# Kernel tuning notes

Measured on AMD Instinct MI355X. Metric: run time of the kernel, lower is better.

## Reference

```python
import jax, jax.numpy as jnp
import numpy as np
from jax.ops import segment_sum, segment_max

B, L, D, H, DK, NL, V, FF = 8, 256, 256, 8, 32, 4, 2048, 1024
N = B * L
EPS = 1e-5


def _ln(x, g, b):
    m = jnp.mean(x, -1, keepdims=True)
    v = jnp.var(x, -1, keepdims=True)
    return (x - m) * jax.lax.rsqrt(v + EPS) * g + b


def setup_inputs() -> dict:
    key = jax.random.key(0)
    ks = list(jax.random.split(key, 16))
    # causal decoder-decoder edges, sorted by destination (DGL 'dd' eids)
    dst_seq = np.repeat(np.arange(L), np.arange(L) + 1)
    src_seq = np.concatenate([np.arange(j + 1) for j in range(L)])
    src = jnp.asarray(np.concatenate([src_seq + b * L for b in range(B)]), jnp.int32)
    dst = jnp.asarray(np.concatenate([dst_seq + b * L for b in range(B)]), jnp.int32)
    tokens = jax.random.randint(ks[0], (N,), 0, V)
    positions = jnp.tile(jnp.arange(L), B)  # tgt[1]
    s = 0.02
    nrm = lambda k, sh: jax.random.normal(k, sh, jnp.float32) * s
    return {
        'tokens': tokens, 'positions': positions, 'src': src, 'dst': dst,
        'value_tab': nrm(ks[1], (V, D)),
        'coord_tab': nrm(ks[2], (3, D)),
        'pos_tab': nrm(ks[3], (L, D)),
        'ln1_g': jnp.ones((NL, D), jnp.float32), 'ln1_b': jnp.zeros((NL, D), jnp.float32),
        'Wq': nrm(ks[4], (NL, D, D)), 'Wk': nrm(ks[5], (NL, D, D)),
        'Wv': nrm(ks[6], (NL, D, D)), 'Wo': nrm(ks[7], (NL, D, D)),
        'ln2_g': jnp.ones((NL, D), jnp.float32), 'ln2_b': jnp.zeros((NL, D), jnp.float32),
        'W1': nrm(ks[8], (NL, D, FF)), 'b1': jnp.zeros((NL, FF), jnp.float32),
        'W2': nrm(ks[9], (NL, FF, D)), 'b2': jnp.zeros((NL, D), jnp.float32),
        'lnf_g': jnp.ones((D,), jnp.float32), 'lnf_b': jnp.zeros((D,), jnp.float32),
        'Wgen': nrm(ks[10], (D, V)), 'bgen': jnp.zeros((V,), jnp.float32),
    }


def reference(tokens, positions, src, dst, value_tab, coord_tab, pos_tab,
              ln1_g, ln1_b, Wq, Wk, Wv, Wo, ln2_g, ln2_b,
              W1, b1, W2, b2, lnf_g, lnf_b, Wgen, bgen):
    # embeddings: value*sqrt(d) + coord(pos%3) + pos(pos//3)
    x = value_tab[tokens] * jnp.sqrt(jnp.float32(D)) \
        + coord_tab[positions % 3] + pos_tab[positions // 3]
    inv_sqrt_dk = 1.0 / jnp.sqrt(jnp.float32(DK))
    for i in range(NL):
        # pre_func: layernorm + qkv projection, split heads
        xn = _ln(x, ln1_g[i], ln1_b[i])
        q = (xn @ Wq[i]).reshape(N, H, DK)
        k = (xn @ Wk[i]).reshape(N, H, DK)
        v = (xn @ Wv[i]).reshape(N, H, DK)
        # apply_edges(u_dot_v): per-edge, per-head score
        score = jnp.einsum('ehd,ehd->eh', k[src], q[dst]) * inv_sqrt_dk  # [E,H]
        # edge_softmax over edges grouped by destination node
        m = jax.lax.stop_gradient(
            segment_max(score, dst, num_segments=N, indices_are_sorted=True))
        a = jnp.exp(score - m[dst])
        denom = segment_sum(a, dst, num_segments=N, indices_are_sorted=True)
        alpha = a / denom[dst]  # [E,H]
        # send_and_recv(u_mul_e -> sum): softmax-weighted aggregation
        z = segment_sum(v[src] * alpha[..., None], dst,
                        num_segments=N, indices_are_sorted=True).reshape(N, D)
        # post_func: output proj + residual, then FFN sublayer
        x = x + z @ Wo[i]
        xn2 = _ln(x, ln2_g[i], ln2_b[i])
        x = x + (jax.nn.relu(xn2 @ W1[i] + b1[i]) @ W2[i] + b2[i])
    x = _ln(x, lnf_g, lnf_b)
    return jax.nn.log_softmax(x @ Wgen + bgen, axis=-1)  # generator
```

## Files before the change

### kernel.cpp

```cpp
#include <hip/hip_runtime.h>
#include <hip/hip_bf16.h>
#include <math.h>

constexpr int B_ = 8, L_ = 256, D_ = 256, H_ = 8, DK_ = 32, NL_ = 4, V_ = 2048, FF_ = 1024;
constexpr int N_ = B_ * L_;
constexpr float EPS_ = 1e-5f;

typedef short bf16x8 __attribute__((ext_vector_type(8)));
typedef float f32x4 __attribute__((ext_vector_type(4)));
typedef _Float16 f16x4 __attribute__((ext_vector_type(4)));

__device__ __forceinline__ short f2b(float f) {
    union { __hip_bfloat16 h; short s; } u;
    u.h = __float2bfloat16(f);
    return u.s;
}

__global__ void embed_kernel(const int* __restrict__ tokens, const int* __restrict__ positions,
                             const float* __restrict__ vtab, const float* __restrict__ ctab,
                             const float* __restrict__ ptab, float* __restrict__ x) {
    int n = blockIdx.x, d = threadIdx.x;
    int tok = tokens[n], p = positions[n];
    x[n * D_ + d] = vtab[tok * D_ + d] * 16.0f + ctab[(p % 3) * D_ + d] + ptab[(p / 3) * D_ + d];
}

__global__ void ln_kernel(const float* __restrict__ x, const float* __restrict__ g,
                          const float* __restrict__ b, short* __restrict__ out) {
    __shared__ float r1[4], r2[4], mv[2];
    int n = blockIdx.x, t = threadIdx.x;
    float v = x[n * D_ + t];
    float s1 = v, s2 = v * v;
#pragma unroll
    for (int off = 32; off; off >>= 1) {
        s1 += __shfl_down(s1, off, 64);
        s2 += __shfl_down(s2, off, 64);
    }
    int w = t >> 6;
    if ((t & 63) == 0) { r1[w] = s1; r2[w] = s2; }
    __syncthreads();
    if (t == 0) {
        float a = r1[0] + r1[1] + r1[2] + r1[3];
        float c = r2[0] + r2[1] + r2[2] + r2[3];
        float mean = a * (1.0f / D_);
        float var = c * (1.0f / D_) - mean * mean;
        mv[0] = mean;
        mv[1] = rsqrtf(var + EPS_);
    }
    __syncthreads();
    out[n * D_ + t] = f2b((v - mv[0]) * mv[1] * g[t] + b[t]);
}

__global__ void transpose_w(const float* __restrict__ src, short* __restrict__ dst, int K, int Nn) {
    __shared__ float tile[32][33];
    int n0 = blockIdx.x * 32, k0 = blockIdx.y * 32;
    size_t base = (size_t)blockIdx.z * K * Nn;
    src += base;
    dst += base;
    int tx = threadIdx.x, ty = threadIdx.y;
#pragma unroll
    for (int i = 0; i < 32; i += 8)
        tile[ty + i][tx] = src[(size_t)(k0 + ty + i) * Nn + n0 + tx];
    __syncthreads();
#pragma unroll
    for (int i = 0; i < 32; i += 8)
        dst[(size_t)(n0 + ty + i) * K + k0 + tx] = f2b(tile[tx][ty + i]);
}

template <int EPI, bool HAS_BIAS>
__device__ __forceinline__ void gemm_body(const short* __restrict__ A, const short* __restrict__ Bt,
                                          const float* __restrict__ bias, float* __restrict__ Cf,
                                          short* __restrict__ Cb, int M, int K, int Nout,
                                          int kbeg, int kend, int kz) {
    __shared__ short As[64][48];
    __shared__ short Bs[64][48];
    int t = threadIdx.x;
    int m0 = blockIdx.x * 64, n0 = blockIdx.y * 64;
    int sr = t >> 2, sc = (t & 3) * 8;
    int lane = t & 63, w = t >> 6;
    int mo = (w & 1) * 32, no = (w >> 1) * 32;
    int quad = lane >> 4, r = lane & 15;
    f32x4 acc00 = {}, acc01 = {}, acc10 = {}, acc11 = {};
    const short* Ap = &A[(size_t)(m0 + sr) * K + sc];
    const short* Bp = &Bt[(size_t)(n0 + sr) * K + sc];
    for (int k0 = kbeg; k0 < kend; k0 += 32) {
        int4 av = *(const int4*)(Ap + k0);
        int4 bv = *(const int4*)(Bp + k0);
        __syncthreads();
        *(int4*)&As[sr][sc] = av;
        *(int4*)&Bs[sr][sc] = bv;
        __syncthreads();
        bf16x8 a0 = *(const bf16x8*)&As[mo + r][quad * 8];
        bf16x8 a1 = *(const bf16x8*)&As[mo + 16 + r][quad * 8];
        bf16x8 b0 = *(const bf16x8*)&Bs[no + r][quad * 8];
        bf16x8 b1 = *(const bf16x8*)&Bs[no + 16 + r][quad * 8];
        acc00 = __builtin_amdgcn_mfma_f32_16x16x32_bf16(a0, b0, acc00, 0, 0, 0);
        acc01 = __builtin_amdgcn_mfma_f32_16x16x32_bf16(a0, b1, acc01, 0, 0, 0);
        acc10 = __builtin_amdgcn_mfma_f32_16x16x32_bf16(a1, b0, acc10, 0, 0, 0);
        acc11 = __builtin_amdgcn_mfma_f32_16x16x32_bf16(a1, b1, acc11, 0, 0, 0);
    }
#pragma unroll
    for (int i = 0; i < 2; ++i) {
#pragma unroll
        for (int j = 0; j < 2; ++j) {
            f32x4 acc = (i == 0) ? (j == 0 ? acc00 : acc01) : (j == 0 ? acc10 : acc11);
            int col = n0 + no + j * 16 + r;
            float bval = HAS_BIAS ? bias[col] : 0.f;
#pragma unroll
            for (int p = 0; p < 4; ++p) {
                int row = m0 + mo + i * 16 + quad * 4 + p;
                float v = acc[p];
                if (EPI == 0) {
                    Cf[(size_t)row * Nout + col] = v;
                } else if (EPI == 1) {
                    Cb[(size_t)row * Nout + col] = f2b(fmaxf(v + bval, 0.f));
                } else if (EPI == 2) {
                    float add = v + ((HAS_BIAS && kz == 0) ? bval : 0.f);
                    atomicAdd(&Cf[(size_t)row * Nout + col], add);
                } else if (EPI == 3) {
                    Cf[(size_t)row * Nout + col] = v + bval;
                } else if (EPI == 4) {
                    Cb[(size_t)row * Nout + col] = f2b(v);
                } else {
                    ((_Float16*)Cb)[(size_t)row * Nout + col] = (_Float16)v;
                }
            }
        }
    }
}

__global__ __launch_bounds__(256) void gemm_qkv(const short* __restrict__ A, const short* __restrict__ wq,
                                                const short* __restrict__ wk, const short* __restrict__ wv,
                                                short* __restrict__ q, short* __restrict__ k,
                                                short* __restrict__ v, int M, int K, int Nout) {
    if (blockIdx.z == 0)
        gemm_body<4, false>(A, wq, nullptr, nullptr, q, M, K, Nout, 0, K, 0);
    else if (blockIdx.z == 1)
        gemm_body<4, false>(A, wk, nullptr, nullptr, k, M, K, Nout, 0, K, 0);
    else
        gemm_body<5, false>(A, wv, nullptr, nullptr, v, M, K, Nout, 0, K, 0);
}

template <int SPLITK, bool HAS_BIAS>
__global__ __launch_bounds__(256) void gemm_accum(const short* __restrict__ A, const short* __restrict__ Bt,
                                                  const float* __restrict__ bias, float* __restrict__ C,
                                                  int M, int K, int Nout) {
    int Kp = K / SPLITK;
    int kz = blockIdx.z;
    gemm_body<2, HAS_BIAS>(A, Bt, bias, C, nullptr, M, K, Nout, kz * Kp, kz * Kp + Kp, kz);
}

__global__ __launch_bounds__(256) void gemm_biasrelu_bf16(const short* __restrict__ A,
                                                          const short* __restrict__ Bt,
                                                          const float* __restrict__ bias,
                                                          short* __restrict__ C, int M, int K, int Nout) {
    gemm_body<1, true>(A, Bt, bias, nullptr, C, M, K, Nout, 0, K, 0);
}

__global__ __launch_bounds__(256) void gemm_bias(const short* __restrict__ A, const short* __restrict__ Bt,
                                                 const float* __restrict__ bias, float* __restrict__ C,
                                                 int M, int K, int Nout) {
    gemm_body<3, true>(A, Bt, bias, C, nullptr, M, K, Nout, 0, K, 0);
}

__global__ __launch_bounds__(64) void attn_kernel(const short* __restrict__ q,
                                                  const short* __restrict__ k,
                                                  const _Float16* __restrict__ v,
                                                  short* __restrict__ z) {
    int blk = blockIdx.x;
    int bh = blk & 63;
    int qt = 15 - (blk >> 6);
    int b = bh >> 3, h = bh & 7;
    int lane = threadIdx.x;
    int r = lane & 15, quad = lane >> 4;
    int row0 = b * L_;

    bf16x8 qf = *(const bf16x8*)&q[(size_t)(row0 + qt * 16 + r) * D_ + h * DK_ + quad * 8];
    f32x4 O0 = {}, O1 = {};
    float mA = -1e30f, den = 0.f;
    int nk = qt + 1;

    bf16x8 kf = *(const bf16x8*)&k[(size_t)(row0 + r) * D_ + h * DK_ + quad * 8];
    f16x4 va, vb;
    {
        const _Float16* vp = v + (size_t)(row0 + quad * 4) * D_ + h * DK_;
#pragma unroll
        for (int i = 0; i < 4; ++i) {
            va[i] = vp[(size_t)i * D_ + r];
            vb[i] = vp[(size_t)i * D_ + 16 + r];
        }
    }
    for (int kt = 0; kt < nk; ++kt) {
        bf16x8 kf_n = kf;
        f16x4 va_n = va, vb_n = vb;
        if (kt + 1 < nk) {
            kf_n = *(const bf16x8*)&k[(size_t)(row0 + (kt + 1) * 16 + r) * D_ + h * DK_ + quad * 8];
            const _Float16* vp = v + (size_t)(row0 + (kt + 1) * 16 + quad * 4) * D_ + h * DK_;
#pragma unroll
            for (int i = 0; i < 4; ++i) {
                va_n[i] = vp[(size_t)i * D_ + r];
                vb_n[i] = vp[(size_t)i * D_ + 16 + r];
            }
        }
        f32x4 zero = {};
        f32x4 s = __builtin_amdgcn_mfma_f32_16x16x32_bf16(kf, qf, zero, 0, 0, 0);
#pragma unroll
        for (int i2 = 0; i2 < 4; ++i2) s[i2] *= 0.17677669529663687f;
        if (kt == qt) {
#pragma unroll
            for (int i2 = 0; i2 < 4; ++i2)
                if (quad * 4 + i2 > r) s[i2] = -1e30f;
        }
        float tmax = fmaxf(fmaxf(s[0], s[1]), fmaxf(s[2], s[3]));
        tmax = fmaxf(tmax, __shfl_xor(tmax, 16, 64));
        tmax = fmaxf(tmax, __shfl_xor(tmax, 32, 64));
        float mn = fmaxf(mA, tmax);
        float alpha = __expf(mA - mn);
        mA = mn;
        float p0 = __expf(s[0] - mn), p1 = __expf(s[1] - mn);
        float p2 = __expf(s[2] - mn), p3 = __expf(s[3] - mn);
        float ts = (p0 + p1) + (p2 + p3);
        ts += __shfl_xor(ts, 16, 64);
        ts += __shfl_xor(ts, 32, 64);
        den = den * alpha + ts;
        f16x4 pf;
        pf[0] = (_Float16)p0; pf[1] = (_Float16)p1; pf[2] = (_Float16)p2; pf[3] = (_Float16)p3;
        float al[4];
#pragma unroll
        for (int i2 = 0; i2 < 4; ++i2) al[i2] = __shfl(alpha, quad * 4 + i2, 64);
#pragma unroll
        for (int i2 = 0; i2 < 4; ++i2) { O0[i2] *= al[i2]; O1[i2] *= al[i2]; }
        O0 = __builtin_amdgcn_mfma_f32_16x16x16f16(pf, va, O0, 0, 0, 0);
        O1 = __builtin_amdgcn_mfma_f32_16x16x16f16(pf, vb, O1, 0, 0, 0);
        kf = kf_n; va = va_n; vb = vb_n;
    }
#pragma unroll
    for (int i2 = 0; i2 < 4; ++i2) {
        float inv = 1.0f / __shfl(den, quad * 4 + i2, 64);
        int rowz = row0 + qt * 16 + quad * 4 + i2;
        z[(size_t)rowz * D_ + h * DK_ + r] = f2b(O0[i2] * inv);
        z[(size_t)rowz * D_ + h * DK_ + 16 + r] = f2b(O1[i2] * inv);
    }
}

__global__ void lsm_kernel(float* __restrict__ logits) {
    __shared__ float rm[4], rs[4];
    int row = blockIdx.x, t = threadIdx.x;
    float* p = logits + (size_t)row * V_;
    float vals[8];
    float mx = -INFINITY;
#pragma unroll
    for (int i = 0; i < 8; ++i) {
        vals[i] = p[t + i * 256];
        mx = fmaxf(mx, vals[i]);
    }
#pragma unroll
    for (int off = 32; off; off >>= 1) mx = fmaxf(mx, __shfl_xor(mx, off, 64));
    int w = t >> 6;
    if ((t & 63) == 0) rm[w] = mx;
    __syncthreads();
    mx = fmaxf(fmaxf(rm[0], rm[1]), fmaxf(rm[2], rm[3]));
    float s = 0.f;
#pragma unroll
    for (int i = 0; i < 8; ++i) s += __expf(vals[i] - mx);
#pragma unroll
    for (int off = 32; off; off >>= 1) s += __shfl_xor(s, off, 64);
    if ((t & 63) == 0) rs[w] = s;
    __syncthreads();
    s = rs[0] + rs[1] + rs[2] + rs[3];
    float lse = mx + logf(s);
#pragma unroll
    for (int i = 0; i < 8; ++i) p[t + i * 256] = vals[i] - lse;
}

extern "C" void kernel_launch(void* const* d_in, const int* in_sizes, int n_in,
                              void* d_out, int out_size, void* d_ws, size_t ws_size,
                              hipStream_t stream) {
    const int* tokens = (const int*)d_in[0];
    const int* positions = (const int*)d_in[1];
    const float* vtab = (const float*)d_in[4];
    const float* ctab = (const float*)d_in[5];
    const float* ptab = (const float*)d_in[6];
    const float* ln1_g = (const float*)d_in[7];
    const float* ln1_b = (const float*)d_in[8];
    const float* Wq = (const float*)d_in[9];
    const float* Wk = (const float*)d_in[10];
    const float* Wv = (const float*)d_in[11];
    const float* Wo = (const float*)d_in[12];
    const float* ln2_g = (const float*)d_in[13];
    const float* ln2_b = (const float*)d_in[14];
    const float* W1 = (const float*)d_in[15];
    const float* b1 = (const float*)d_in[16];
    const float* W2 = (const float*)d_in[17];
    const float* b2 = (const float*)d_in[18];
    const float* lnf_g = (const float*)d_in[19];
    const float* lnf_b = (const float*)d_in[20];
    const float* Wgen = (const float*)d_in[21];
    const float* bgen = (const float*)d_in[22];

    char* p = (char*)d_ws;
    float* x = (float*)p;      p += (size_t)N_ * D_ * 4;
    short* qb = (short*)p;     p += (size_t)N_ * D_ * 4;
    short* kb = (short*)p;     p += (size_t)N_ * D_ * 4;
    short* vbh = (short*)p;    p += (size_t)N_ * D_ * 4;
    short* xnb = (short*)p;    p += (size_t)N_ * D_ * 2;
    short* zbb = (short*)p;    p += (size_t)N_ * D_ * 2;
    short* hbb = (short*)p;    p += (size_t)N_ * FF_ * 2;
    short* wqT = (short*)p;    p += (size_t)NL_ * D_ * D_ * 2;
    short* wkT = (short*)p;    p += (size_t)NL_ * D_ * D_ * 2;
    short* wvT = (short*)p;    p += (size_t)NL_ * D_ * D_ * 2;
    short* woT = (short*)p;    p += (size_t)NL_ * D_ * D_ * 2;
    short* w1T = (short*)p;    p += (size_t)NL_ * D_ * FF_ * 2;
    short* w2T = (short*)p;    p += (size_t)NL_ * FF_ * D_ * 2;
    short* wgT = (short*)p;    p += (size_t)D_ * V_ * 2;
    float* out = (float*)d_out;

    dim3 tb(32, 8);
    transpose_w<<<dim3(8, 8, NL_), tb, 0, stream>>>(Wq, wqT, D_, D_);
    transpose_w<<<dim3(8, 8, NL_), tb, 0, stream>>>(Wk, wkT, D_, D_);
    transpose_w<<<dim3(8, 8, NL_), tb, 0, stream>>>(Wv, wvT, D_, D_);
    transpose_w<<<dim3(8, 8, NL_), tb, 0, stream>>>(Wo, woT, D_, D_);
    transpose_w<<<dim3(32, 8, NL_), tb, 0, stream>>>(W1, w1T, D_, FF_);
    transpose_w<<<dim3(8, 32, NL_), tb, 0, stream>>>(W2, w2T, FF_, D_);
    transpose_w<<<dim3(64, 8, 1), tb, 0, stream>>>(Wgen, wgT, D_, V_);

    embed_kernel<<<N_, 256, 0, stream>>>(tokens, positions, vtab, ctab, ptab, x);
    dim3 gQKV(N_ / 64, D_ / 64, 3);
    dim3 gWo(N_ / 64, D_ / 64, 2);
    dim3 gW1(N_ / 64, FF_ / 64);
    dim3 gW2(N_ / 64, D_ / 64, 4);
    dim3 gGen(N_ / 64, V_ / 64);
    for (int i = 0; i < NL_; ++i) {
        ln_kernel<<<N_, 256, 0, stream>>>(x, ln1_g + i * D_, ln1_b + i * D_, xnb);
        gemm_qkv<<<gQKV, 256, 0, stream>>>(xnb, wqT + (size_t)i * D_ * D_, wkT + (size_t)i * D_ * D_,
                                           wvT + (size_t)i * D_ * D_, qb, kb, vbh, N_, D_, D_);
        attn_kernel<<<B_ * H_ * 16, 64, 0, stream>>>(qb, kb, (const _Float16*)vbh, zbb);
        gemm_accum<2, false><<<gWo, 256, 0, stream>>>(zbb, woT + (size_t)i * D_ * D_, nullptr, x, N_, D_, D_);
        ln_kernel<<<N_, 256, 0, stream>>>(x, ln2_g + i * D_, ln2_b + i * D_, xnb);
        gemm_biasrelu_bf16<<<gW1, 256, 0, stream>>>(xnb, w1T + (size_t)i * D_ * FF_, b1 + (size_t)i * FF_,
                                                    hbb, N_, D_, FF_);
        gemm_accum<4, true><<<gW2, 256, 0, stream>>>(hbb, w2T + (size_t)i * FF_ * D_, b2 + (size_t)i * D_,
                                                     x, N_, FF_, D_);
    }
    ln_kernel<<<N_, 256, 0, stream>>>(x, lnf_g, lnf_b, xnb);
    gemm_bias<<<gGen, 256, 0, stream>>>(xnb, wgT, bgen, out, N_, D_, V_);
    lsm_kernel<<<N_, 256, 0, stream>>>(out);
}
```

Before: 335.1 us.

## Stage full K-chunks in registers for GEMMs and fuse weight transposes

The GEMM body now loads its whole K slice (up to 256 elements) into registers up front and stages it into wider LDS tiles in 128-wide phases. This replaces a 32-wide step that needed two barriers per step, so the loop drops many syncs and global-load latency stalls. The seven transpose launches become one combined kernel, and the embedding is fused with the first layernorm. The cost is more registers and more LDS per block, which may lower occupancy.

```diff
diff --git a/kernel.cpp b/kernel.cpp
--- a/kernel.cpp
+++ b/kernel.cpp
@@ -16,19 +16,16 @@
     return u.s;
 }
 
-__global__ void embed_kernel(const int* __restrict__ tokens, const int* __restrict__ positions,
-                             const float* __restrict__ vtab, const float* __restrict__ ctab,
-                             const float* __restrict__ ptab, float* __restrict__ x) {
-    int n = blockIdx.x, d = threadIdx.x;
-    int tok = tokens[n], p = positions[n];
-    x[n * D_ + d] = vtab[tok * D_ + d] * 16.0f + ctab[(p % 3) * D_ + d] + ptab[(p / 3) * D_ + d];
-}
-
-__global__ void ln_kernel(const float* __restrict__ x, const float* __restrict__ g,
-                          const float* __restrict__ b, short* __restrict__ out) {
+__global__ void embed_ln_kernel(const int* __restrict__ tokens, const int* __restrict__ positions,
+                                const float* __restrict__ vtab, const float* __restrict__ ctab,
+                                const float* __restrict__ ptab, const float* __restrict__ g,
+                                const float* __restrict__ b, float* __restrict__ x,
+                                short* __restrict__ out) {
     __shared__ float r1[4], r2[4], mv[2];
     int n = blockIdx.x, t = threadIdx.x;
-    float v = x[n * D_ + t];
+    int tok = tokens[n], p = positions[n];
+    float v = vtab[tok * D_ + t] * 16.0f + ctab[(p % 3) * D_ + t] + ptab[(p / 3) * D_ + t];
+    x[n * D_ + t] = v;
     float s1 = v, s2 = v * v;
 #pragma unroll
     for (int off = 32; off; off >>= 1) {
@@ -50,29 +47,87 @@
     out[n * D_ + t] = f2b((v - mv[0]) * mv[1] * g[t] + b[t]);
 }
 
-__global__ void transpose_w(const float* __restrict__ src, short* __restrict__ dst, int K, int Nn) {
+__global__ void ln_kernel(const float* __restrict__ x, const float* __restrict__ g,
+                          const float* __restrict__ b, short* __restrict__ out) {
+    __shared__ float r1[4], r2[4], mv[2];
+    int n = blockIdx.x, t = threadIdx.x;
+    float v = x[n * D_ + t];
+    float s1 = v, s2 = v * v;
+#pragma unroll
+    for (int off = 32; off; off >>= 1) {
+        s1 += __shfl_down(s1, off, 64);
+        s2 += __shfl_down(s2, off, 64);
+    }
+    int w = t >> 6;
+    if ((t & 63) == 0) { r1[w] = s1; r2[w] = s2; }
+    __syncthreads();
+    if (t == 0) {
+        float a = r1[0] + r1[1] + r1[2] + r1[3];
+        float c = r2[0] + r2[1] + r2[2] + r2[3];
+        float mean = a * (1.0f / D_);
+        float var = c * (1.0f / D_) - mean * mean;
+        mv[0] = mean;
+        mv[1] = rsqrtf(var + EPS_);
+    }
+    __syncthreads();
+    out[n * D_ + t] = f2b((v - mv[0]) * mv[1] * g[t] + b[t]);
+}
+
+__global__ void transpose_all(const float* __restrict__ Wq, const float* __restrict__ Wk,
+                              const float* __restrict__ Wv, const float* __restrict__ Wo,
+                              const float* __restrict__ W1, const float* __restrict__ W2,
+                              const float* __restrict__ Wgen,
+                              short* __restrict__ wqT, short* __restrict__ wkT,
+                              short* __restrict__ wvT, short* __restrict__ woT,
+                              short* __restrict__ w1T, short* __restrict__ w2T,
+                              short* __restrict__ wgT) {
     __shared__ float tile[32][33];
-    int n0 = blockIdx.x * 32, k0 = blockIdx.y * 32;
-    size_t base = (size_t)blockIdx.z * K * Nn;
-    src += base;
-    dst += base;
-    int tx = threadIdx.x, ty = threadIdx.y;
+    int id = blockIdx.x;
+    const float* src;
+    short* dst;
+    int K, Nn, tx, ty;
+    if (id < 1024) {
+        int m = id >> 8, rem = id & 255, layer = rem >> 6, tt = rem & 63;
+        K = 256; Nn = 256; tx = tt & 7; ty = tt >> 3;
+        size_t off = (size_t)layer * 256 * 256;
+        if (m == 0) { src = Wq + off; dst = wqT + off; }
+        else if (m == 1) { src = Wk + off; dst = wkT + off; }
+        else if (m == 2) { src = Wv + off; dst = wvT + off; }
+        else { src = Wo + off; dst = woT + off; }
+    } else if (id < 2048) {
+        int rem = id - 1024, layer = rem >> 8, tt = rem & 255;
+        K = 256; Nn = 1024; tx = tt & 31; ty = tt >> 5;
+        size_t off = (size_t)layer * 256 * 1024;
+        src = W1 + off; dst = w1T + off;
+    } else if (id < 3072) {
+        int rem = id - 2048, layer = rem >> 8, tt = rem & 255;
+        K = 1024; Nn = 256; tx = tt & 7; ty = tt >> 3;
+        size_t off = (size_t)layer * 1024 * 256;
+        src = W2 + off; dst = w2T + off;
+    } else {
+        int tt = id - 3072;
+        K = 256; Nn = 2048; tx = tt & 63; ty = tt >> 6;
+        src = Wgen; dst = wgT;
+    }
+    int n0 = tx * 32, k0 = ty * 32;
+    int x_ = threadIdx.x, y_ = threadIdx.y;
 #pragma unroll
     for (int i = 0; i < 32; i += 8)
-        tile[ty + i][tx] = src[(size_t)(k0 + ty + i) * Nn + n0 + tx];
+        tile[y_ + i][x_] = src[(size_t)(k0 + y_ + i) * Nn + n0 + x_];
     __syncthreads();
 #pragma unroll
     for (int i = 0; i < 32; i += 8)
-        dst[(size_t)(n0 + ty + i) * K + k0 + tx] = f2b(tile[tx][ty + i]);
-}
-
-template <int EPI, bool HAS_BIAS>
+        dst[(size_t)(n0 + y_ + i) * K + k0 + x_] = f2b(tile[x_][y_ + i]);
+}
+
+template <int EPI, bool HAS_BIAS, int NC>
 __device__ __forceinline__ void gemm_body(const short* __restrict__ A, const short* __restrict__ Bt,
                                           const float* __restrict__ bias, float* __restrict__ Cf,
                                           short* __restrict__ Cb, int M, int K, int Nout,
-                                          int kbeg, int kend, int kz) {
-    __shared__ short As[64][48];
-    __shared__ short Bs[64][48];
+                                          int kbeg, int kz) {
+    constexpr int LDW = 136;
+    __shared__ short As[64][LDW];
+    __shared__ short Bs[64][LDW];
     int t = threadIdx.x;
     int m0 = blockIdx.x * 64, n0 = blockIdx.y * 64;
     int sr = t >> 2, sc = (t & 3) * 8;
@@ -80,23 +135,34 @@
     int mo = (w & 1) * 32, no = (w >> 1) * 32;
     int quad = lane >> 4, r = lane & 15;
     f32x4 acc00 = {}, acc01 = {}, acc10 = {}, acc11 = {};
-    const short* Ap = &A[(size_t)(m0 + sr) * K + sc];
-    const short* Bp = &Bt[(size_t)(n0 + sr) * K + sc];
-    for (int k0 = kbeg; k0 < kend; k0 += 32) {
-        int4 av = *(const int4*)(Ap + k0);
-        int4 bv = *(const int4*)(Bp + k0);
+    const short* Ap = &A[(size_t)(m0 + sr) * K + kbeg + sc];
+    const short* Bp = &Bt[(size_t)(n0 + sr) * K + kbeg + sc];
+    int4 ar[NC], br[NC];
+#pragma unroll
+    for (int c = 0; c < NC; ++c) ar[c] = *(const int4*)(Ap + c * 32);
+#pragma unroll
+    for (int c = 0; c < NC; ++c) br[c] = *(const int4*)(Bp + c * 32);
+    constexpr int NPH = NC / 4;
+#pragma unroll
+    for (int ph = 0; ph < NPH; ++ph) {
+        if (ph) __syncthreads();
+#pragma unroll
+        for (int c = 0; c < 4; ++c) {
+            *(int4*)&As[sr][c * 32 + sc] = ar[ph * 4 + c];
+            *(int4*)&Bs[sr][c * 32 + sc] = br[ph * 4 + c];
+        }
         __syncthreads();
-        *(int4*)&As[sr][sc] = av;
-        *(int4*)&Bs[sr][sc] = bv;
-        __syncthreads();
-        bf16x8 a0 = *(const bf16x8*)&As[mo + r][quad * 8];
-        bf16x8 a1 = *(const bf16x8*)&As[mo + 16 + r][quad * 8];
-        bf16x8 b0 = *(const bf16x8*)&Bs[no + r][quad * 8];
-        bf16x8 b1 = *(const bf16x8*)&Bs[no + 16 + r][quad * 8];
-        acc00 = __builtin_amdgcn_mfma_f32_16x16x32_bf16(a0, b0, acc00, 0, 0, 0);
-        acc01 = __builtin_amdgcn_mfma_f32_16x16x32_bf16(a0, b1, acc01, 0, 0, 0);
-        acc10 = __builtin_amdgcn_mfma_f32_16x16x32_bf16(a1, b0, acc10, 0, 0, 0);
-        acc11 = __builtin_amdgcn_mfma_f32_16x16x32_bf16(a1, b1, acc11, 0, 0, 0);
+#pragma unroll
+        for (int c = 0; c < 4; ++c) {
+            bf16x8 a0 = *(const bf16x8*)&As[mo + r][c * 32 + quad * 8];
+            bf16x8 a1 = *(const bf16x8*)&As[mo + 16 + r][c * 32 + quad * 8];
+            bf16x8 b0 = *(const bf16x8*)&Bs[no + r][c * 32 + quad * 8];
+            bf16x8 b1 = *(const bf16x8*)&Bs[no + 16 + r][c * 32 + quad * 8];
+            acc00 = __builtin_amdgcn_mfma_f32_16x16x32_bf16(a0, b0, acc00, 0, 0, 0);
+            acc01 = __builtin_amdgcn_mfma_f32_16x16x32_bf16(a0, b1, acc01, 0, 0, 0);
+            acc10 = __builtin_amdgcn_mfma_f32_16x16x32_bf16(a1, b0, acc10, 0, 0, 0);
+            acc11 = __builtin_amdgcn_mfma_f32_16x16x32_bf16(a1, b1, acc11, 0, 0, 0);
+        }
     }
 #pragma unroll
     for (int i = 0; i < 2; ++i) {
@@ -133,33 +199,33 @@
                                                 short* __restrict__ q, short* __restrict__ k,
                                                 short* __restrict__ v, int M, int K, int Nout) {
     if (blockIdx.z == 0)
-        gemm_body<4, false>(A, wq, nullptr, nullptr, q, M, K, Nout, 0, K, 0);
+        gemm_body<4, false, 8>(A, wq, nullptr, nullptr, q, M, K, Nout, 0, 0);
     else if (blockIdx.z == 1)
-        gemm_body<4, false>(A, wk, nullptr, nullptr, k, M, K, Nout, 0, K, 0);
+        gemm_body<4, false, 8>(A, wk, nullptr, nullptr, k, M, K, Nout, 0, 0);
     else
-        gemm_body<5, false>(A, wv, nullptr, nullptr, v, M, K, Nout, 0, K, 0);
-}
-
-template <int SPLITK, bool HAS_BIAS>
+        gemm_body<5, false, 8>(A, wv, nullptr, nullptr, v, M, K, Nout, 0, 0);
+}
+
+template <int SPLITK, bool HAS_BIAS, int NC>
 __global__ __launch_bounds__(256) void gemm_accum(const short* __restrict__ A, const short* __restrict__ Bt,
                                                   const float* __restrict__ bias, float* __restrict__ C,
                                                   int M, int K, int Nout) {
     int Kp = K / SPLITK;
     int kz = blockIdx.z;
-    gemm_body<2, HAS_BIAS>(A, Bt, bias, C, nullptr, M, K, Nout, kz * Kp, kz * Kp + Kp, kz);
+    gemm_body<2, HAS_BIAS, NC>(A, Bt, bias, C, nullptr, M, K, Nout, kz * Kp, kz);
 }
 
 __global__ __launch_bounds__(256) void gemm_biasrelu_bf16(const short* __restrict__ A,
                                                           const short* __restrict__ Bt,
                                                           const float* __restrict__ bias,
                                                           short* __restrict__ C, int M, int K, int Nout) {
-    gemm_body<1, true>(A, Bt, bias, nullptr, C, M, K, Nout, 0, K, 0);
+    gemm_body<1, true, 8>(A, Bt, bias, nullptr, C, M, K, Nout, 0, 0);
 }
 
 __global__ __launch_bounds__(256) void gemm_bias(const short* __restrict__ A, const short* __restrict__ Bt,
                                                  const float* __restrict__ bias, float* __restrict__ C,
                                                  int M, int K, int Nout) {
-    gemm_body<3, true>(A, Bt, bias, C, nullptr, M, K, Nout, 0, K, 0);
+    gemm_body<3, true, 8>(A, Bt, bias, C, nullptr, M, K, Nout, 0, 0);
 }
 
 __global__ __launch_bounds__(64) void attn_kernel(const short* __restrict__ q,
@@ -315,31 +381,28 @@
     float* out = (float*)d_out;
 
     dim3 tb(32, 8);
-    transpose_w<<<dim3(8, 8, NL_), tb, 0, stream>>>(Wq, wqT, D_, D_);
-    transpose_w<<<dim3(8, 8, NL_), tb, 0, stream>>>(Wk, wkT, D_, D_);
-    transpose_w<<<dim3(8, 8, NL_), tb, 0, stream>>>(Wv, wvT, D_, D_);
-    transpose_w<<<dim3(8, 8, NL_), tb, 0, stream>>>(Wo, woT, D_, D_);
-    transpose_w<<<dim3(32, 8, NL_), tb, 0, stream>>>(W1, w1T, D_, FF_);
-    transpose_w<<<dim3(8, 32, NL_), tb, 0, stream>>>(W2, w2T, FF_, D_);
-    transpose_w<<<dim3(64, 8, 1), tb, 0, stream>>>(Wgen, wgT, D_, V_);
-
-    embed_kernel<<<N_, 256, 0, stream>>>(tokens, positions, vtab, ctab, ptab, x);
+    transpose_all<<<3584, tb, 0, stream>>>(Wq, Wk, Wv, Wo, W1, W2, Wgen,
+                                           wqT, wkT, wvT, woT, w1T, w2T, wgT);
+
+    embed_ln_kernel<<<N_, 256, 0, stream>>>(tokens, positions, vtab, ctab, ptab,
+                                            ln1_g, ln1_b, x, xnb);
     dim3 gQKV(N_ / 64, D_ / 64, 3);
     dim3 gWo(N_ / 64, D_ / 64, 2);
     dim3 gW1(N_ / 64, FF_ / 64);
     dim3 gW2(N_ / 64, D_ / 64, 4);
     dim3 gGen(N_ / 64, V_ / 64);
     for (int i = 0; i < NL_; ++i) {
-        ln_kernel<<<N_, 256, 0, stream>>>(x, ln1_g + i * D_, ln1_b + i * D_, xnb);
+        if (i > 0)
+            ln_kernel<<<N_, 256, 0, stream>>>(x, ln1_g + i * D_, ln1_b + i * D_, xnb);
         gemm_qkv<<<gQKV, 256, 0, stream>>>(xnb, wqT + (size_t)i * D_ * D_, wkT + (size_t)i * D_ * D_,
                                            wvT + (size_t)i * D_ * D_, qb, kb, vbh, N_, D_, D_);
         attn_kernel<<<B_ * H_ * 16, 64, 0, stream>>>(qb, kb, (const _Float16*)vbh, zbb);
-        gemm_accum<2, false><<<gWo, 256, 0, stream>>>(zbb, woT + (size_t)i * D_ * D_, nullptr, x, N_, D_, D_);
+        gemm_accum<2, false, 4><<<gWo, 256, 0, stream>>>(zbb, woT + (size_t)i * D_ * D_, nullptr, x, N_, D_, D_);
         ln_kernel<<<N_, 256, 0, stream>>>(x, ln2_g + i * D_, ln2_b + i * D_, xnb);
         gemm_biasrelu_bf16<<<gW1, 256, 0, stream>>>(xnb, w1T + (size_t)i * D_ * FF_, b1 + (size_t)i * FF_,
                                                     hbb, N_, D_, FF_);
-        gemm_accum<4, true><<<gW2, 256, 0, stream>>>(hbb, w2T + (size_t)i * FF_ * D_, b2 + (size_t)i * D_,
-                                                     x, N_, FF_, D_);
+        gemm_accum<4, true, 8><<<gW2, 256, 0, stream>>>(hbb, w2T + (size_t)i * FF_ * D_, b2 + (size_t)i * D_,
+                                                        x, N_, FF_, D_);
     }
     ln_kernel<<<N_, 256, 0, stream>>>(x, lnf_g, lnf_b, xnb);
     gemm_bias<<<gGen, 256, 0, stream>>>(xnb, wgT, bgen, out, N_, D_, V_);
```

After: 414.9 us. 1.24x slower.

## Fuse layernorm into GEMM prologues, merge weight transposes, prefetch next K tile

Applied to the files above, without the earlier changes.

Removes the standalone layernorm kernels. Each GEMM block now loads fp32 rows of x, computes the row mean and variance with 4-lane shuffles, and packs normalized bf16 A-tiles in registers before the MFMA loop. The seven weight-transpose launches are merged into one kernel, and the GEMM K loop now loads the next tile's global data before the current tile's compute. The trade-off is that LN is recomputed once per N-tile (16 or 32 times for the wide GEMMs), and the 64-float register array may raise register pressure and lower occupancy.

```diff
diff --git a/kernel.cpp b/kernel.cpp
--- a/kernel.cpp
+++ b/kernel.cpp
@@ -24,46 +24,91 @@
     x[n * D_ + d] = vtab[tok * D_ + d] * 16.0f + ctab[(p % 3) * D_ + d] + ptab[(p / 3) * D_ + d];
 }
 
-__global__ void ln_kernel(const float* __restrict__ x, const float* __restrict__ g,
-                          const float* __restrict__ b, short* __restrict__ out) {
-    __shared__ float r1[4], r2[4], mv[2];
-    int n = blockIdx.x, t = threadIdx.x;
-    float v = x[n * D_ + t];
-    float s1 = v, s2 = v * v;
-#pragma unroll
-    for (int off = 32; off; off >>= 1) {
-        s1 += __shfl_down(s1, off, 64);
-        s2 += __shfl_down(s2, off, 64);
-    }
-    int w = t >> 6;
-    if ((t & 63) == 0) { r1[w] = s1; r2[w] = s2; }
+__global__ void transpose_all(const float* __restrict__ Wq, const float* __restrict__ Wk,
+                              const float* __restrict__ Wv, const float* __restrict__ Wo,
+                              const float* __restrict__ W1, const float* __restrict__ W2,
+                              const float* __restrict__ Wgen,
+                              short* __restrict__ wqT, short* __restrict__ wkT,
+                              short* __restrict__ wvT, short* __restrict__ woT,
+                              short* __restrict__ w1T, short* __restrict__ w2T,
+                              short* __restrict__ wgT) {
+    __shared__ float tile[32][33];
+    int id = blockIdx.x;
+    const float* src;
+    short* dst;
+    int K, Nn, tx, ty;
+    if (id < 1024) {
+        int m = id >> 8, rem = id & 255, layer = rem >> 6, tt = rem & 63;
+        K = 256; Nn = 256; tx = tt & 7; ty = tt >> 3;
+        size_t off = (size_t)layer * 256 * 256;
+        if (m == 0) { src = Wq + off; dst = wqT + off; }
+        else if (m == 1) { src = Wk + off; dst = wkT + off; }
+        else if (m == 2) { src = Wv + off; dst = wvT + off; }
+        else { src = Wo + off; dst = woT + off; }
+    } else if (id < 2048) {
+        int rem = id - 1024, layer = rem >> 8, tt = rem & 255;
+        K = 256; Nn = 1024; tx = tt & 31; ty = tt >> 5;
+        size_t off = (size_t)layer * 256 * 1024;
+        src = W1 + off; dst = w1T + off;
+    } else if (id < 3072) {
+        int rem = id - 2048, layer = rem >> 8, tt = rem & 255;
+        K = 1024; Nn = 256; tx = tt & 7; ty = tt >> 3;
+        size_t off = (size_t)layer * 1024 * 256;
+        src = W2 + off; dst = w2T + off;
+    } else {
+        int tt = id - 3072;
+        K = 256; Nn = 2048; tx = tt & 63; ty = tt >> 6;
+        src = Wgen; dst = wgT;
+    }
+    int n0 = tx * 32, k0 = ty * 32;
+    int x_ = threadIdx.x, y_ = threadIdx.y;
+#pragma unroll
+    for (int i = 0; i < 32; i += 8)
+        tile[y_ + i][x_] = src[(size_t)(k0 + y_ + i) * Nn + n0 + x_];
     __syncthreads();
-    if (t == 0) {
-        float a = r1[0] + r1[1] + r1[2] + r1[3];
-        float c = r2[0] + r2[1] + r2[2] + r2[3];
-        float mean = a * (1.0f / D_);
-        float var = c * (1.0f / D_) - mean * mean;
-        mv[0] = mean;
-        mv[1] = rsqrtf(var + EPS_);
-    }
-    __syncthreads();
-    out[n * D_ + t] = f2b((v - mv[0]) * mv[1] * g[t] + b[t]);
-}
-
-__global__ void transpose_w(const float* __restrict__ src, short* __restrict__ dst, int K, int Nn) {
-    __shared__ float tile[32][33];
-    int n0 = blockIdx.x * 32, k0 = blockIdx.y * 32;
-    size_t base = (size_t)blockIdx.z * K * Nn;
-    src += base;
-    dst += base;
-    int tx = threadIdx.x, ty = threadIdx.y;
 #pragma unroll
     for (int i = 0; i < 32; i += 8)
-        tile[ty + i][tx] = src[(size_t)(k0 + ty + i) * Nn + n0 + tx];
-    __syncthreads();
-#pragma unroll
-    for (int i = 0; i < 32; i += 8)
-        dst[(size_t)(n0 + ty + i) * K + k0 + tx] = f2b(tile[tx][ty + i]);
+        dst[(size_t)(n0 + y_ + i) * K + k0 + x_] = f2b(tile[x_][y_ + i]);
+}
+
+__device__ __forceinline__ int4 pack8(const float* v) {
+    union { short s[8]; int4 q; } u;
+#pragma unroll
+    for (int j = 0; j < 8; ++j) u.s[j] = f2b(v[j]);
+    return u.q;
+}
+
+template <int EPI, bool HAS_BIAS>
+__device__ __forceinline__ void gemm_epilogue(f32x4 acc00, f32x4 acc01, f32x4 acc10, f32x4 acc11,
+                                              const float* __restrict__ bias, float* __restrict__ Cf,
+                                              short* __restrict__ Cb, int Nout, int kz,
+                                              int m0, int n0, int mo, int no, int quad, int r) {
+#pragma unroll
+    for (int i = 0; i < 2; ++i) {
+#pragma unroll
+        for (int j = 0; j < 2; ++j) {
+            f32x4 acc = (i == 0) ? (j == 0 ? acc00 : acc01) : (j == 0 ? acc10 : acc11);
+            int col = n0 + no + j * 16 + r;
+            float bval = HAS_BIAS ? bias[col] : 0.f;
+#pragma unroll
+            for (int p = 0; p < 4; ++p) {
+                int row = m0 + mo + i * 16 + quad * 4 + p;
+                float v = acc[p];
+                if (EPI == 1) {
+                    Cb[(size_t)row * Nout + col] = f2b(fmaxf(v + bval, 0.f));
+                } else if (EPI == 2) {
+                    float add = v + ((HAS_BIAS && kz == 0) ? bval : 0.f);
+                    atomicAdd(&Cf[(size_t)row * Nout + col], add);
+                } else if (EPI == 3) {
+                    Cf[(size_t)row * Nout + col] = v + bval;
+                } else if (EPI == 4) {
+                    Cb[(size_t)row * Nout + col] = f2b(v);
+                } else {
+                    ((_Float16*)Cb)[(size_t)row * Nout + col] = (_Float16)v;
+                }
+            }
+        }
+    }
 }
 
 template <int EPI, bool HAS_BIAS>
@@ -82,9 +127,14 @@
     f32x4 acc00 = {}, acc01 = {}, acc10 = {}, acc11 = {};
     const short* Ap = &A[(size_t)(m0 + sr) * K + sc];
     const short* Bp = &Bt[(size_t)(n0 + sr) * K + sc];
+    int4 av = *(const int4*)(Ap + kbeg);
+    int4 bv = *(const int4*)(Bp + kbeg);
     for (int k0 = kbeg; k0 < kend; k0 += 32) {
-        int4 av = *(const int4*)(Ap + k0);
-        int4 bv = *(const int4*)(Bp + k0);
+        int4 an = av, bn = bv;
+        if (k0 + 32 < kend) {
+            an = *(const int4*)(Ap + k0 + 32);
+            bn = *(const int4*)(Bp + k0 + 32);
+        }
         __syncthreads();
         *(int4*)&As[sr][sc] = av;
         *(int4*)&Bs[sr][sc] = bv;
@@ -97,47 +147,111 @@
         acc01 = __builtin_amdgcn_mfma_f32_16x16x32_bf16(a0, b1, acc01, 0, 0, 0);
         acc10 = __builtin_amdgcn_mfma_f32_16x16x32_bf16(a1, b0, acc10, 0, 0, 0);
         acc11 = __builtin_amdgcn_mfma_f32_16x16x32_bf16(a1, b1, acc11, 0, 0, 0);
-    }
-#pragma unroll
-    for (int i = 0; i < 2; ++i) {
-#pragma unroll
-        for (int j = 0; j < 2; ++j) {
-            f32x4 acc = (i == 0) ? (j == 0 ? acc00 : acc01) : (j == 0 ? acc10 : acc11);
-            int col = n0 + no + j * 16 + r;
-            float bval = HAS_BIAS ? bias[col] : 0.f;
-#pragma unroll
-            for (int p = 0; p < 4; ++p) {
-                int row = m0 + mo + i * 16 + quad * 4 + p;
-                float v = acc[p];
-                if (EPI == 0) {
-                    Cf[(size_t)row * Nout + col] = v;
-                } else if (EPI == 1) {
-                    Cb[(size_t)row * Nout + col] = f2b(fmaxf(v + bval, 0.f));
-                } else if (EPI == 2) {
-                    float add = v + ((HAS_BIAS && kz == 0) ? bval : 0.f);
-                    atomicAdd(&Cf[(size_t)row * Nout + col], add);
-                } else if (EPI == 3) {
-                    Cf[(size_t)row * Nout + col] = v + bval;
-                } else if (EPI == 4) {
-                    Cb[(size_t)row * Nout + col] = f2b(v);
-                } else {
-                    ((_Float16*)Cb)[(size_t)row * Nout + col] = (_Float16)v;
-                }
-            }
-        }
-    }
-}
-
-__global__ __launch_bounds__(256) void gemm_qkv(const short* __restrict__ A, const short* __restrict__ wq,
-                                                const short* __restrict__ wk, const short* __restrict__ wv,
-                                                short* __restrict__ q, short* __restrict__ k,
-                                                short* __restrict__ v, int M, int K, int Nout) {
+        av = an; bv = bn;
+    }
+    gemm_epilogue<EPI, HAS_BIAS>(acc00, acc01, acc10, acc11, bias, Cf, Cb, Nout, kz,
+                                 m0, n0, mo, no, quad, r);
+}
+
+template <int EPI, bool HAS_BIAS>
+__device__ __forceinline__ void gemm_ln_body(const float* __restrict__ X,
+                                             const float* __restrict__ lg, const float* __restrict__ lb,
+                                             const short* __restrict__ Bt,
+                                             const float* __restrict__ bias, float* __restrict__ Cf,
+                                             short* __restrict__ Cb, int Nout) {
+    __shared__ short As[64][48];
+    __shared__ short Bs[64][48];
+    __shared__ float gs[256], bs[256];
+    int t = threadIdx.x;
+    int m0 = blockIdx.x * 64, n0 = blockIdx.y * 64;
+    int sr = t >> 2, sc = (t & 3) * 8;
+    int lane = t & 63, w = t >> 6;
+    int mo = (w & 1) * 32, no = (w >> 1) * 32;
+    int quad = lane >> 4, r = lane & 15;
+
+    float xv[64];
+    const float* xp = &X[(size_t)(m0 + sr) * 256 + sc];
+#pragma unroll
+    for (int c = 0; c < 8; ++c) {
+        *(float4*)&xv[c * 8] = *(const float4*)(xp + c * 32);
+        *(float4*)&xv[c * 8 + 4] = *(const float4*)(xp + c * 32 + 4);
+    }
+    const short* Bp = &Bt[(size_t)(n0 + sr) * 256 + sc];
+    int4 bv = *(const int4*)Bp;
+    gs[t] = lg[t];
+    bs[t] = lb[t];
+
+    float s1 = 0.f, s2 = 0.f;
+#pragma unroll
+    for (int j = 0; j < 64; ++j) {
+        s1 += xv[j];
+        s2 += xv[j] * xv[j];
+    }
+    s1 += __shfl_xor(s1, 1, 64); s1 += __shfl_xor(s1, 2, 64);
+    s2 += __shfl_xor(s2, 1, 64); s2 += __shfl_xor(s2, 2, 64);
+    float mean = s1 * (1.0f / 256.0f);
+    float inv = rsqrtf(s2 * (1.0f / 256.0f) - mean * mean + EPS_);
+    __syncthreads();
+
+    int4 a_regs[8];
+#pragma unroll
+    for (int c = 0; c < 8; ++c) {
+        float tmp[8];
+#pragma unroll
+        for (int j = 0; j < 8; ++j)
+            tmp[j] = (xv[c * 8 + j] - mean) * inv * gs[c * 32 + sc + j] + bs[c * 32 + sc + j];
+        a_regs[c] = pack8(tmp);
+    }
+
+    f32x4 acc00 = {}, acc01 = {}, acc10 = {}, acc11 = {};
+#pragma unroll
+    for (int c = 0; c < 8; ++c) {
+        int4 bn = bv;
+        if (c < 7) bn = *(const int4*)(Bp + (c + 1) * 32);
+        __syncthreads();
+        *(int4*)&As[sr][sc] = a_regs[c];
+        *(int4*)&Bs[sr][sc] = bv;
+        __syncthreads();
+        bf16x8 a0 = *(const bf16x8*)&As[mo + r][quad * 8];
+        bf16x8 a1 = *(const bf16x8*)&As[mo + 16 + r][quad * 8];
+        bf16x8 b0 = *(const bf16x8*)&Bs[no + r][quad * 8];
+        bf16x8 b1 = *(const bf16x8*)&Bs[no + 16 + r][quad * 8];
+        acc00 = __builtin_amdgcn_mfma_f32_16x16x32_bf16(a0, b0, acc00, 0, 0, 0);
+        acc01 = __builtin_amdgcn_mfma_f32_16x16x32_bf16(a0, b1, acc01, 0, 0, 0);
+        acc10 = __builtin_amdgcn_mfma_f32_16x16x32_bf16(a1, b0, acc10, 0, 0, 0);
+        acc11 = __builtin_amdgcn_mfma_f32_16x16x32_bf16(a1, b1, acc11, 0, 0, 0);
+        bv = bn;
+    }
+    gemm_epilogue<EPI, HAS_BIAS>(acc00, acc01, acc10, acc11, bias, Cf, Cb, Nout, 0,
+                                 m0, n0, mo, no, quad, r);
+}
+
+__global__ __launch_bounds__(256) void gemm_ln_qkv(const float* __restrict__ X,
+                                                   const float* __restrict__ lg, const float* __restrict__ lb,
+                                                   const short* __restrict__ wq, const short* __restrict__ wk,
+                                                   const short* __restrict__ wv,
+                                                   short* __restrict__ q, short* __restrict__ k,
+                                                   short* __restrict__ v) {
     if (blockIdx.z == 0)
-        gemm_body<4, false>(A, wq, nullptr, nullptr, q, M, K, Nout, 0, K, 0);
+        gemm_ln_body<4, false>(X, lg, lb, wq, nullptr, nullptr, q, D_);
     else if (blockIdx.z == 1)
-        gemm_body<4, false>(A, wk, nullptr, nullptr, k, M, K, Nout, 0, K, 0);
+        gemm_ln_body<4, false>(X, lg, lb, wk, nullptr, nullptr, k, D_);
     else
-        gemm_body<5, false>(A, wv, nullptr, nullptr, v, M, K, Nout, 0, K, 0);
+        gemm_ln_body<5, false>(X, lg, lb, wv, nullptr, nullptr, v, D_);
+}
+
+__global__ __launch_bounds__(256) void gemm_ln_relu(const float* __restrict__ X,
+                                                    const float* __restrict__ lg, const float* __restrict__ lb,
+                                                    const short* __restrict__ Bt, const float* __restrict__ bias,
+                                                    short* __restrict__ C) {
+    gemm_ln_body<1, true>(X, lg, lb, Bt, bias, nullptr, C, FF_);
+}
+
+__global__ __launch_bounds__(256) void gemm_ln_bias(const float* __restrict__ X,
+                                                    const float* __restrict__ lg, const float* __restrict__ lb,
+                                                    const short* __restrict__ Bt, const float* __restrict__ bias,
+                                                    float* __restrict__ C) {
+    gemm_ln_body<3, true>(X, lg, lb, Bt, bias, C, nullptr, V_);
 }
 
 template <int SPLITK, bool HAS_BIAS>
@@ -147,19 +261,6 @@
     int Kp = K / SPLITK;
     int kz = blockIdx.z;
     gemm_body<2, HAS_BIAS>(A, Bt, bias, C, nullptr, M, K, Nout, kz * Kp, kz * Kp + Kp, kz);
-}
-
-__global__ __launch_bounds__(256) void gemm_biasrelu_bf16(const short* __restrict__ A,
-                                                          const short* __restrict__ Bt,
-                                                          const float* __restrict__ bias,
-                                                          short* __restrict__ C, int M, int K, int Nout) {
-    gemm_body<1, true>(A, Bt, bias, nullptr, C, M, K, Nout, 0, K, 0);
-}
-
-__global__ __launch_bounds__(256) void gemm_bias(const short* __restrict__ A, const short* __restrict__ Bt,
-                                                 const float* __restrict__ bias, float* __restrict__ C,
-                                                 int M, int K, int Nout) {
-    gemm_body<3, true>(A, Bt, bias, C, nullptr, M, K, Nout, 0, K, 0);
 }
 
 __global__ __launch_bounds__(64) void attn_kernel(const short* __restrict__ q,
@@ -302,7 +403,6 @@
     short* qb = (short*)p;     p += (size_t)N_ * D_ * 4;
     short* kb = (short*)p;     p += (size_t)N_ * D_ * 4;
     short* vbh = (short*)p;    p += (size_t)N_ * D_ * 4;
-    short* xnb = (short*)p;    p += (size_t)N_ * D_ * 2;
     short* zbb = (short*)p;    p += (size_t)N_ * D_ * 2;
     short* hbb = (short*)p;    p += (size_t)N_ * FF_ * 2;
     short* wqT = (short*)p;    p += (size_t)NL_ * D_ * D_ * 2;
@@ -315,33 +415,27 @@
     float* out = (float*)d_out;
 
     dim3 tb(32, 8);
-    transpose_w<<<dim3(8, 8, NL_), tb, 0, stream>>>(Wq, wqT, D_, D_);
-    transpose_w<<<dim3(8, 8, NL_), tb, 0, stream>>>(Wk, wkT, D_, D_);
-    transpose_w<<<dim3(8, 8, NL_), tb, 0, stream>>>(Wv, wvT, D_, D_);
-    transpose_w<<<dim3(8, 8, NL_), tb, 0, stream>>>(Wo, woT, D_, D_);
-    transpose_w<<<dim3(32, 8, NL_), tb, 0, stream>>>(W1, w1T, D_, FF_);
-    transpose_w<<<dim3(8, 32, NL_), tb, 0, stream>>>(W2, w2T, FF_, D_);
-    transpose_w<<<dim3(64, 8, 1), tb, 0, stream>>>(Wgen, wgT, D_, V_);
+    transpose_all<<<3584, tb, 0, stream>>>(Wq, Wk, Wv, Wo, W1, W2, Wgen,
+                                           wqT, wkT, wvT, woT, w1T, w2T, wgT);
 
     embed_kernel<<<N_, 256, 0, stream>>>(tokens, positions, vtab, ctab, ptab, x);
+
     dim3 gQKV(N_ / 64, D_ / 64, 3);
     dim3 gWo(N_ / 64, D_ / 64, 2);
     dim3 gW1(N_ / 64, FF_ / 64);
     dim3 gW2(N_ / 64, D_ / 64, 4);
     dim3 gGen(N_ / 64, V_ / 64);
     for (int i = 0; i < NL_; ++i) {
-        ln_kernel<<<N_, 256, 0, stream>>>(x, ln1_g + i * D_, ln1_b + i * D_, xnb);
-        gemm_qkv<<<gQKV, 256, 0, stream>>>(xnb, wqT + (size_t)i * D_ * D_, wkT + (size_t)i * D_ * D_,
-                                           wvT + (size_t)i * D_ * D_, qb, kb, vbh, N_, D_, D_);
+        gemm_ln_qkv<<<gQKV, 256, 0, stream>>>(x, ln1_g + i * D_, ln1_b + i * D_,
+                                              wqT + (size_t)i * D_ * D_, wkT + (size_t)i * D_ * D_,
+                                              wvT + (size_t)i * D_ * D_, qb, kb, vbh);
         attn_kernel<<<B_ * H_ * 16, 64, 0, stream>>>(qb, kb, (const _Float16*)vbh, zbb);
         gemm_accum<2, false><<<gWo, 256, 0, stream>>>(zbb, woT + (size_t)i * D_ * D_, nullptr, x, N_, D_, D_);
-        ln_kernel<<<N_, 256, 0, stream>>>(x, ln2_g + i * D_, ln2_b + i * D_, xnb);
-        gemm_biasrelu_bf16<<<gW1, 256, 0, stream>>>(xnb, w1T + (size_t)i * D_ * FF_, b1 + (size_t)i * FF_,
-                                                    hbb, N_, D_, FF_);
+        gemm_ln_relu<<<gW1, 256, 0, stream>>>(x, ln2_g + i * D_, ln2_b + i * D_,
+                                              w1T + (size_t)i * D_ * FF_, b1 + (size_t)i * FF_, hbb);
         gemm_accum<4, true><<<gW2, 256, 0, stream>>>(hbb, w2T + (size_t)i * FF_ * D_, b2 + (size_t)i * D_,
                                                      x, N_, FF_, D_);
     }
-    ln_kernel<<<N_, 256, 0, stream>>>(x, lnf_g, lnf_b, xnb);
-    gemm_bias<<<gGen, 256, 0, stream>>>(xnb, wgT, bgen, out, N_, D_, V_);
+    gemm_ln_bias<<<gGen, 256, 0, stream>>>(x, lnf_g, lnf_b, wgT, bgen, out);
     lsm_kernel<<<N_, 256, 0, stream>>>(out);
 }
```

New measurement: 308.7 us. -7.9%, faster.
